# Performance work log

Hardware: AMD Instinct MI355X
Metric: run time of the kernel (lower is better)

Reference implementation:

```python
import jax, jax.numpy as jnp
import numpy as np

TAU = 2.0          # LIF membrane time constant (decay_input=True)
V_TH = 1.0         # spike threshold, hard reset to 0
SG_ALPHA = 2.0     # ATan surrogate gradient alpha

@jax.custom_vjp
def spike(x):
    # Heaviside spike with ATan surrogate gradient
    return (x >= 0).astype(x.dtype)

def _spike_fwd(x):
    return spike(x), x

def _spike_bwd(x, g):
    sg = (SG_ALPHA / 2.0) / (1.0 + (jnp.pi / 2.0 * SG_ALPHA * x) ** 2)
    return (g * sg,)

spike.defvjp(_spike_fwd, _spike_bwd)

def setup_inputs() -> dict:
    key = jax.random.key(0)
    ks = jax.random.split(key, 12)
    B, T, D_IN, H, D_OUT = 256, 250, 700, 128, 20
    def lin(k, fan_in, fan_out):
        bound = 1.0 / np.sqrt(fan_in)
        kw, kb = jax.random.split(k)
        W = jax.random.uniform(kw, (fan_in, fan_out), jnp.float32, -bound, bound)
        b = jax.random.uniform(kb, (fan_out,), jnp.float32, -bound, bound)
        return W, b
    W1, b1 = lin(ks[0], D_IN, H)
    rcW1, rcb1 = lin(ks[1], H, H)
    W2, b2 = lin(ks[2], H, H)
    rcW2, rcb2 = lin(ks[3], H, H)
    W3, b3 = lin(ks[4], H, D_OUT)
    x = jax.random.normal(ks[5], (B, T, D_IN), jnp.float32)
    return {"x": x, "W1": W1, "b1": b1, "rcW1": rcW1, "rcb1": rcb1,
            "W2": W2, "b2": b2, "rcW2": rcW2, "rcb2": rcb2,
            "W3": W3, "b3": b3}

def _lif(v, u):
    # decay_input LIF: v += (u - v)/tau ; spike ; hard reset to 0
    v = v + (u - v) / TAU
    s = spike(v - V_TH)
    v = v * (1.0 - s)
    return v, s

def reference(x, W1, b1, rcW1, rcb1, W2, b2, rcW2, rcb2, W3, b3):
    B = x.shape[0]
    H = W1.shape[1]
    xt = jnp.swapaxes(x, 0, 1)  # [T, B, D_in] — matches permute(1,0,2)

    def step(carry, x_t):
        y1, v1, y2, v2, acc = carry
        h1 = x_t @ W1 + b1                      # first Linear
        u1 = y1 @ rcW1 + rcb1 + h1              # recurrent container 1
        v1, y1 = _lif(v1, u1)
        h2 = y1 @ W2 + b2                       # mid Linear
        u2 = y2 @ rcW2 + rcb2 + h2              # recurrent container 2
        v2, y2 = _lif(v2, u2)
        out_t = y2 @ W3 + b3                    # readout
        return (y1, v1, y2, v2, acc + out_t), None

    z = jnp.zeros((B, H), x.dtype)
    acc0 = jnp.zeros((B, W3.shape[1]), x.dtype)
    (y1, v1, y2, v2, acc), _ = jax.lax.scan(step, (z, z, z, z, acc0), xt)
    return acc  # res.sum(0): [B, out_dim]
```

## Files before the change

kernel.cpp:

```cpp
#include <hip/hip_runtime.h>
#include <cstdint>
#include <cstddef>

#define Bb   256
#define Tt   250
#define DIN  700
#define Hh   128
#define DOUT 20

constexpr int BM  = 128;
constexpr int BK  = 20;
constexpr int BN  = 128;
constexpr int BMP = BM + 4;

__device__ __forceinline__ int bswz(int g) { return g ^ (g >> 3); }

__global__ __launch_bounds__(256, 2) void gemm_h1(const float* __restrict__ x,
                                                  const float* __restrict__ W1,
                                                  const float* __restrict__ b1,
                                                  float* __restrict__ H1) {
    __shared__ float Ast[BK][BMP];
    __shared__ float Bs[BK][BN];

    const int tid = threadIdx.x;
    const int tx  = tid & 15;
    const int ty  = tid >> 4;
    const int m0  = blockIdx.x * BM;

    const int c0 = bswz(tx * 2) * 4;
    const int c1 = bswz(tx * 2 + 1) * 4;

    float acc[8][8];
#pragma unroll
    for (int r = 0; r < 8; ++r)
#pragma unroll
        for (int c = 0; c < 8; ++c) acc[r][c] = 0.f;

    for (int k0 = 0; k0 < DIN; k0 += BK) {
#pragma unroll
        for (int idx = tid; idx < 640; idx += 256) {
            int row = idx / 5;
            int kq  = (idx - row * 5) * 4;
            const float4 v =
                *(const float4*)&x[(size_t)(m0 + row) * DIN + (k0 + kq)];
            Ast[kq + 0][row] = v.x;
            Ast[kq + 1][row] = v.y;
            Ast[kq + 2][row] = v.z;
            Ast[kq + 3][row] = v.w;
        }
#pragma unroll
        for (int idx = tid; idx < 640; idx += 256) {
            int kr = idx >> 5;
            int g  = idx & 31;
            *(float4*)&Bs[kr][bswz(g) * 4] =
                *(const float4*)&W1[(size_t)(k0 + kr) * BN + g * 4];
        }
        __syncthreads();

#pragma unroll
        for (int kk = 0; kk < BK; ++kk) {
            float a[8], bv[8];
            *(float4*)&a[0]  = *(const float4*)&Ast[kk][ty * 8];
            *(float4*)&a[4]  = *(const float4*)&Ast[kk][ty * 8 + 4];
            *(float4*)&bv[0] = *(const float4*)&Bs[kk][c0];
            *(float4*)&bv[4] = *(const float4*)&Bs[kk][c1];
#pragma unroll
            for (int r = 0; r < 8; ++r)
#pragma unroll
                for (int c = 0; c < 8; ++c)
                    acc[r][c] = fmaf(a[r], bv[c], acc[r][c]);
        }
        __syncthreads();
    }

    float bb[8];
#pragma unroll
    for (int c = 0; c < 8; ++c) bb[c] = b1[tx * 8 + c];

#pragma unroll
    for (int r = 0; r < 8; ++r) {
        size_t row = (size_t)(m0 + ty * 8 + r);
        float4 o0, o1;
        o0.x = acc[r][0] + bb[0]; o0.y = acc[r][1] + bb[1];
        o0.z = acc[r][2] + bb[2]; o0.w = acc[r][3] + bb[3];
        o1.x = acc[r][4] + bb[4]; o1.y = acc[r][5] + bb[5];
        o1.z = acc[r][6] + bb[6]; o1.w = acc[r][7] + bb[7];
        *(float4*)&H1[row * Hh + tx * 8]     = o0;
        *(float4*)&H1[row * Hh + tx * 8 + 4] = o1;
    }
}


#define WAITV(N)                                                       \
    asm volatile("s_waitcnt vmcnt(" #N ")" ::: "memory");              \
    __builtin_amdgcn_sched_barrier(0)

__device__ __forceinline__ void gll16(const void* g, void* l) {
    __builtin_amdgcn_global_load_lds(
        (const __attribute__((address_space(1))) uint32_t*)g,
        (__attribute__((address_space(3))) uint32_t*)l, 16, 0, 0);
}

__device__ __forceinline__ void issue_chunk(const char* hg, char* ringb,
                                            int c, int n) {
    const char* g = hg + (size_t)c * 4096;
    char* l = ringb + (c & 3) * 4096;
    for (int i = 0; i < n; ++i) gll16(g + (size_t)i * 1024, l + i * 1024);
}

#define EXTR(K)                                                        \
    if (mlo) { K = (int)__ffsll(mlo) - 1; mlo &= mlo - 1ull; }         \
    else     { K = 64 + (int)__ffsll(mhi) - 1; mhi &= mhi - 1ull; }
#define EXTR2(K)                                                       \
    if (mlo)      { K = (int)__ffsll(mlo) - 1; mlo &= mlo - 1ull; }    \
    else if (mhi) { K = 64 + (int)__ffsll(mhi) - 1; mhi &= mhi - 1ull; }

#define GATHER4(D0X, D0Y, D1X, D1Y, D2X, D2Y, D3X, D3Y, P0, P1, P2, P3)       \
    asm volatile("global_load_dword %0, %8, off\n\t"                          \
                 "global_load_dword %1, %8, off offset:256\n\t"               \
                 "global_load_dword %2, %9, off\n\t"                          \
                 "global_load_dword %3, %9, off offset:256\n\t"               \
                 "global_load_dword %4, %10, off\n\t"                         \
                 "global_load_dword %5, %10, off offset:256\n\t"              \
                 "global_load_dword %6, %11, off\n\t"                         \
                 "global_load_dword %7, %11, off offset:256\n\t"              \
                 "s_waitcnt vmcnt(0)"                                         \
                 : "=&v"(D0X), "=&v"(D0Y), "=&v"(D1X), "=&v"(D1Y),            \
                   "=&v"(D2X), "=&v"(D2Y), "=&v"(D3X), "=&v"(D3Y)             \
                 : "v"(P0), "v"(P1), "v"(P2), "v"(P3)                         \
                 : "memory");

__global__ __launch_bounds__(64) void recurrent(
    const float* __restrict__ H1,   const float* __restrict__ rcW1,
    const float* __restrict__ rcb1, const float* __restrict__ W2,
    const float* __restrict__ b2,   const float* __restrict__ rcW2,
    const float* __restrict__ rcb2, const float* __restrict__ W3,
    const float* __restrict__ b3,   float* __restrict__ out) {

    __shared__ float ring[32 * Hh];

    const int lane = threadIdx.x;
    const int b    = blockIdx.x;

    const float rcb1x = rcb1[lane], rcb1y = rcb1[lane + 64];
    const float bb2x  = b2[lane]      + rcb2[lane];
    const float bb2y  = b2[lane + 64] + rcb2[lane + 64];
    const float* __restrict__ h1p = H1 + (size_t)b * Tt * Hh;

    const char* hg = (const char*)h1p + lane * 16;
    char* ringb = (char*)ring;
    issue_chunk(hg, ringb, 0, 4);
    issue_chunk(hg, ringb, 1, 4);
    issue_chunk(hg, ringb, 2, 4);
    WAITV(4);

    float v1x = 0.f, v1y = 0.f, v2x = 0.f, v2y = 0.f;
    float cntx = 0.f, cnty = 0.f;
    float u1gx = 0.f, u1gy = 0.f;
    float u2gx = 0.f, u2gy = 0.f;
    bool  sp1 = false, sp2 = false;

    float h1xs[4], h1ys[4];
#pragma unroll
    for (int j = 0; j < 4; ++j) {
        h1xs[j] = ring[(j << 7) + lane];
        h1ys[j] = ring[(j << 7) + lane + 64];
    }

#define STEP(T, J)                                                            \
    {                                                                         \
        const int t_ = (T);                                                   \
           \
        float u1xv = h1xs[J] + rcb1x;                                         \
        float u1yv = h1ys[J] + rcb1y;                                         \
        if (sp1) { u1xv += u1gx; u1yv += u1gy; }                              \
        int tp = t_ + 4; tp = (tp < Tt) ? tp : (Tt - 1);                      \
        const float* rp_ = &ring[(tp & 31) << 7];                             \
        h1xs[J] = rp_[lane];                                                  \
        h1ys[J] = rp_[lane + 64];                                             \
        v1x = v1x + (u1xv - v1x) * 0.5f;                                      \
        v1y = v1y + (u1yv - v1y) * 0.5f;                                      \
        const bool s1x = (v1x >= 1.0f);                                       \
        const bool s1y = (v1y >= 1.0f);                                       \
        if (s1x) v1x = 0.f;                                                   \
        if (s1y) v1y = 0.f;                                                   \
        const unsigned long long a0 = __ballot((int)s1x);                     \
        const unsigned long long a1 = __ballot((int)s1y);                     \
                  \
        float uW2x = 0.f, uW2y = 0.f;                                         \
        sp1 = ((a0 | a1) != 0ull);                                            \
        if (sp1) {                                                            \
            float g1x = 0.f, g1y = 0.f;                                       \
            unsigned long long mlo = a0, mhi = a1;                            \
            while (mlo | mhi) {                                               \
                int k0; int k1 = -1;                                          \
                EXTR(k0) EXTR2(k1)                                            \
                const int kb = (k1 >= 0 ? k1 : k0);                           \
                const float* pw0 = W2   + ((size_t)k0 << 7) + lane;           \
                const float* pr0 = rcW1 + ((size_t)k0 << 7) + lane;           \
                const float* pw1 = W2   + ((size_t)kb << 7) + lane;           \
                const float* pr1 = rcW1 + ((size_t)kb << 7) + lane;           \
                float w0x, w0y, r0x, r0y, w1x, w1y, r1x, r1y;                 \
                GATHER4(w0x, w0y, r0x, r0y, w1x, w1y, r1x, r1y,               \
                        pw0, pr0, pw1, pr1)                                   \
                uW2x += w0x; uW2y += w0y; g1x += r0x; g1y += r0y;             \
                if (k1 >= 0) {                                                \
                    uW2x += w1x; uW2y += w1y; g1x += r1x; g1y += r1y;         \
                }                                                             \
            }                                                                 \
            u1gx = g1x; u1gy = g1y;                                           \
        }                                                                     \
           \
        float u2xv = bb2x + uW2x;                                             \
        float u2yv = bb2y + uW2y;                                             \
        if (sp2) { u2xv += u2gx; u2yv += u2gy; }                              \
        v2x = v2x + (u2xv - v2x) * 0.5f;                                      \
        v2y = v2y + (u2yv - v2y) * 0.5f;                                      \
        const bool s2x = (v2x >= 1.0f);                                       \
        const bool s2y = (v2y >= 1.0f);                                       \
        if (s2x) v2x = 0.f;                                                   \
        if (s2y) v2y = 0.f;                                                   \
        cntx += s2x ? 1.f : 0.f;                                              \
        cnty += s2y ? 1.f : 0.f;                                              \
        const unsigned long long c0m = __ballot((int)s2x);                    \
        const unsigned long long c1m = __ballot((int)s2y);                    \
          \
        sp2 = ((c0m | c1m) != 0ull);                                          \
        if (sp2) {                                                            \
            float sx = 0.f, sy = 0.f;                                         \
            unsigned long long mlo = c0m, mhi = c1m;                          \
            while (mlo | mhi) {                                               \
                int k0; int k1 = -1; int k2 = -1; int k3 = -1;                \
                EXTR(k0) EXTR2(k1) EXTR2(k2) EXTR2(k3)                        \
                const float* p0 = rcW2 + ((size_t)k0 << 7) + lane;            \
                const float* p1 =                                             \
                    rcW2 + ((size_t)(k1 >= 0 ? k1 : k0) << 7) + lane;         \
                const float* p2 =                                             \
                    rcW2 + ((size_t)(k2 >= 0 ? k2 : k0) << 7) + lane;         \
                const float* p3 =                                             \
                    rcW2 + ((size_t)(k3 >= 0 ? k3 : k0) << 7) + lane;         \
                float d0x, d0y, d1x, d1y, d2x, d2y, d3x, d3y;                 \
                GATHER4(d0x, d0y, d1x, d1y, d2x, d2y, d3x, d3y,               \
                        p0, p1, p2, p3)                                       \
                sx += d0x; sy += d0y;                                         \
                if (k1 >= 0) { sx += d1x; sy += d1y; }                        \
                if (k2 >= 0) { sx += d2x; sy += d2y; }                        \
                if (k3 >= 0) { sx += d3x; sy += d3y; }                        \
            }                                                                 \
            u2gx = sx; u2gy = sy;                                             \
        }                                                                     \
    }

#pragma unroll 1
    for (int c = 0; c < 31; ++c) {
        if (c <= 27)      issue_chunk(hg, ringb, c + 3, 4);
        else if (c == 28) issue_chunk(hg, ringb, 31, 1);
        if (c <= 27) { WAITV(8); } else { WAITV(0); }
        const int t0 = c << 3;
#pragma unroll 1
        for (int g = 0; g < 2; ++g) {
            const int t = t0 + (g << 2);
            STEP(t + 0, 0)
            STEP(t + 1, 1)
            STEP(t + 2, 2)
            STEP(t + 3, 3)
        }
    }
    WAITV(0);
    STEP(248, 0)
    STEP(249, 1)
#undef STEP

    __syncthreads();
    ring[lane]      = cntx;
    ring[lane + 64] = cnty;
    __syncthreads();
    if (lane < DOUT) {
        float o = (float)Tt * b3[lane];
#pragma unroll 8
        for (int k = 0; k < Hh; ++k) o += ring[k] * W3[k * DOUT + lane];
        out[b * DOUT + lane] = o;
    }
}

extern "C" void kernel_launch(void* const* d_in, const int* in_sizes, int n_in,
                              void* d_out, int out_size, void* d_ws, size_t ws_size,
                              hipStream_t stream) {
    const float* x    = (const float*)d_in[0];
    const float* W1   = (const float*)d_in[1];
    const float* b1   = (const float*)d_in[2];
    const float* rcW1 = (const float*)d_in[3];
    const float* rcb1 = (const float*)d_in[4];
    const float* W2   = (const float*)d_in[5];
    const float* b2   = (const float*)d_in[6];
    const float* rcW2 = (const float*)d_in[7];
    const float* rcb2 = (const float*)d_in[8];
    const float* W3   = (const float*)d_in[9];
    const float* b3   = (const float*)d_in[10];

    float* out = (float*)d_out;
    float* H1  = (float*)d_ws;

    gemm_h1<<<(Bb * Tt) / BM, 256, 0, stream>>>(x, W1, b1, H1);
    recurrent<<<Bb, 64, 0, stream>>>(H1, rcW1, rcb1, W2, b2, rcW2, rcb2, W3,
                                     b3, out);
}
```

Measured before the change: 450.9 us.

## Preload whole H1 sequence into LDS with 512 threads before recurrence

Replaces the async ring-buffer streaming of H1 (global_load_lds chunks with vmcnt waits inside the time loop) with a bulk cooperative copy of the entire 250x128 H1 slice into 125 KB of shared memory by 512 threads. A single wavefront then runs the recurrence reading only from LDS, with no waitcnt stalls inside the loop. The cost is a serial preload phase before the recurrence starts, with no overlap. The large LDS footprint also limits residency to one block per CU, and seven of the eight wavefronts sit idle during the recurrence.

```diff
diff --git a/kernel.cpp b/kernel.cpp
--- a/kernel.cpp
+++ b/kernel.cpp
@@ -90,23 +90,6 @@
     }
 }
 
-
-#define WAITV(N)                                                       \
-    asm volatile("s_waitcnt vmcnt(" #N ")" ::: "memory");              \
-    __builtin_amdgcn_sched_barrier(0)
-
-__device__ __forceinline__ void gll16(const void* g, void* l) {
-    __builtin_amdgcn_global_load_lds(
-        (const __attribute__((address_space(1))) uint32_t*)g,
-        (__attribute__((address_space(3))) uint32_t*)l, 16, 0, 0);
-}
-
-__device__ __forceinline__ void issue_chunk(const char* hg, char* ringb,
-                                            int c, int n) {
-    const char* g = hg + (size_t)c * 4096;
-    char* l = ringb + (c & 3) * 4096;
-    for (int i = 0; i < n; ++i) gll16(g + (size_t)i * 1024, l + i * 1024);
-}
 
 #define EXTR(K)                                                        \
     if (mlo) { K = (int)__ffsll(mlo) - 1; mlo &= mlo - 1ull; }         \
@@ -130,52 +113,56 @@
                  : "v"(P0), "v"(P1), "v"(P2), "v"(P3)                         \
                  : "memory");
 
-__global__ __launch_bounds__(64) void recurrent(
+__global__ __launch_bounds__(512) void recurrent(
     const float* __restrict__ H1,   const float* __restrict__ rcW1,
     const float* __restrict__ rcb1, const float* __restrict__ W2,
     const float* __restrict__ b2,   const float* __restrict__ rcW2,
     const float* __restrict__ rcb2, const float* __restrict__ W3,
     const float* __restrict__ b3,   float* __restrict__ out) {
 
-    __shared__ float ring[32 * Hh];
-
-    const int lane = threadIdx.x;
-    const int b    = blockIdx.x;
-
-    const float rcb1x = rcb1[lane], rcb1y = rcb1[lane + 64];
-    const float bb2x  = b2[lane]      + rcb2[lane];
-    const float bb2y  = b2[lane + 64] + rcb2[lane + 64];
-    const float* __restrict__ h1p = H1 + (size_t)b * Tt * Hh;
-
-    const char* hg = (const char*)h1p + lane * 16;
-    char* ringb = (char*)ring;
-    issue_chunk(hg, ringb, 0, 4);
-    issue_chunk(hg, ringb, 1, 4);
-    issue_chunk(hg, ringb, 2, 4);
-    WAITV(4);
-
-    float v1x = 0.f, v1y = 0.f, v2x = 0.f, v2y = 0.f;
-    float cntx = 0.f, cnty = 0.f;
-    float u1gx = 0.f, u1gy = 0.f;
-    float u2gx = 0.f, u2gy = 0.f;
-    bool  sp1 = false, sp2 = false;
-
-    float h1xs[4], h1ys[4];
-#pragma unroll
-    for (int j = 0; j < 4; ++j) {
-        h1xs[j] = ring[(j << 7) + lane];
-        h1ys[j] = ring[(j << 7) + lane + 64];
-    }
+    __shared__ __align__(16) float h1ls[Tt * Hh];
+
+    const int tid = threadIdx.x;
+    const int b   = blockIdx.x;
+
+    {
+        const float4* __restrict__ src =
+            (const float4*)(H1 + (size_t)b * Tt * Hh);
+        float4* dst = (float4*)h1ls;
+#pragma unroll 4
+        for (int i = tid; i < (Tt * Hh / 4); i += 512) dst[i] = src[i];
+    }
+    __syncthreads();
+
+    if (tid < 64) {
+        const int lane = tid;
+
+        const float rcb1x = rcb1[lane], rcb1y = rcb1[lane + 64];
+        const float bb2x  = b2[lane]      + rcb2[lane];
+        const float bb2y  = b2[lane + 64] + rcb2[lane + 64];
+
+        float v1x = 0.f, v1y = 0.f, v2x = 0.f, v2y = 0.f;
+        float cntx = 0.f, cnty = 0.f;
+        float u1gx = 0.f, u1gy = 0.f;
+        float u2gx = 0.f, u2gy = 0.f;
+        bool  sp1 = false, sp2 = false;
+
+        float h1xs[4], h1ys[4];
+#pragma unroll
+        for (int j = 0; j < 4; ++j) {
+            h1xs[j] = h1ls[(j << 7) + lane];
+            h1ys[j] = h1ls[(j << 7) + lane + 64];
+        }
 
 #define STEP(T, J)                                                            \
     {                                                                         \
         const int t_ = (T);                                                   \
-           \
+            \
         float u1xv = h1xs[J] + rcb1x;                                         \
         float u1yv = h1ys[J] + rcb1y;                                         \
         if (sp1) { u1xv += u1gx; u1yv += u1gy; }                              \
         int tp = t_ + 4; tp = (tp < Tt) ? tp : (Tt - 1);                      \
-        const float* rp_ = &ring[(tp & 31) << 7];                             \
+        const float* rp_ = &h1ls[tp << 7];                                    \
         h1xs[J] = rp_[lane];                                                  \
         h1ys[J] = rp_[lane + 64];                                             \
         v1x = v1x + (u1xv - v1x) * 0.5f;                                      \
@@ -186,7 +173,7 @@
         if (s1y) v1y = 0.f;                                                   \
         const unsigned long long a0 = __ballot((int)s1x);                     \
         const unsigned long long a1 = __ballot((int)s1y);                     \
-                  \
+            \
         float uW2x = 0.f, uW2y = 0.f;                                         \
         sp1 = ((a0 | a1) != 0ull);                                            \
         if (sp1) {                                                            \
@@ -224,7 +211,7 @@
         cnty += s2y ? 1.f : 0.f;                                              \
         const unsigned long long c0m = __ballot((int)s2x);                    \
         const unsigned long long c1m = __ballot((int)s2y);                    \
-          \
+            \
         sp2 = ((c0m | c1m) != 0ull);                                          \
         if (sp2) {                                                            \
             float sx = 0.f, sy = 0.f;                                         \
@@ -252,34 +239,27 @@
     }
 
 #pragma unroll 1
-    for (int c = 0; c < 31; ++c) {
-        if (c <= 27)      issue_chunk(hg, ringb, c + 3, 4);
-        else if (c == 28) issue_chunk(hg, ringb, 31, 1);
-        if (c <= 27) { WAITV(8); } else { WAITV(0); }
-        const int t0 = c << 3;
-#pragma unroll 1
-        for (int g = 0; g < 2; ++g) {
-            const int t = t0 + (g << 2);
+        for (int g = 0; g < 62; ++g) {
+            const int t = g << 2;
             STEP(t + 0, 0)
             STEP(t + 1, 1)
             STEP(t + 2, 2)
             STEP(t + 3, 3)
         }
-    }
-    WAITV(0);
-    STEP(248, 0)
-    STEP(249, 1)
+        STEP(248, 0)
+        STEP(249, 1)
 #undef STEP
 
+        h1ls[lane]      = cntx;
+        h1ls[lane + 64] = cnty;
+    }
     __syncthreads();
-    ring[lane]      = cntx;
-    ring[lane + 64] = cnty;
-    __syncthreads();
-    if (lane < DOUT) {
-        float o = (float)Tt * b3[lane];
+
+    if (tid < DOUT) {
+        float o = (float)Tt * b3[tid];
 #pragma unroll 8
-        for (int k = 0; k < Hh; ++k) o += ring[k] * W3[k * DOUT + lane];
-        out[b * DOUT + lane] = o;
+        for (int k = 0; k < Hh; ++k) o += h1ls[k] * W3[k * DOUT + tid];
+        out[b * DOUT + tid] = o;
     }
 }
 
@@ -302,6 +282,6 @@
     float* H1  = (float*)d_ws;
 
     gemm_h1<<<(Bb * Tt) / BM, 256, 0, stream>>>(x, W1, b1, H1);
-    recurrent<<<Bb, 64, 0, stream>>>(H1, rcW1, rcb1, W2, b2, rcW2, rcb2, W3,
-                                     b3, out);
+    recurrent<<<Bb, 512, 0, stream>>>(H1, rcW1, rcb1, W2, b2, rcW2, rcb2, W3,
+                                      b3, out);
 }
```

Result: no change. 452.3 us (+0.3%).
